# Kernel tuning notes

Measured on AMD Instinct MI355X. Metric: run time of the kernel, lower is better.

Reference implementation:

```python
import jax, jax.numpy as jnp
import numpy as np

VALUES_PER_ITEM = 4  # 2-bit packed -> 4 values per uint8


def setup_inputs() -> dict:
    key = jax.random.key(0)
    k1, k2, k3 = jax.random.split(key, 3)
    x = jax.random.normal(k1, (4, 4096, 2048), dtype=jnp.float32)
    # packed uint8 weights, stored as int32 with values in [0, 256)
    weight_packed = jax.random.randint(k2, (512, 2048), 0, 256, dtype=jnp.int32)
    weight_scale = jnp.ones((1,), dtype=jnp.float32)
    bias = jax.random.normal(k3, (2048,), dtype=jnp.float32) * 0.01
    return {"x": x, "weight_packed": weight_packed,
            "weight_scale": weight_scale, "bias": bias}


def unpack_weights_bitnet(packed, dtype):
    # packed: [out//4, in]. HF BitNet layout: group i occupies rows
    # [i*out//4 : (i+1)*out//4], extracted from bits (2i, 2i+1), minus 1.
    parts = [((packed >> (2 * i)) & 3) for i in range(VALUES_PER_ITEM)]
    return jnp.concatenate(parts, axis=0).astype(dtype) - 1.0  # [out, in]


def activation_quant(x, num_bits=8):
    qn = -(2 ** (num_bits - 1))          # -128
    qp = 2 ** (num_bits - 1) - 1         # 127
    amax = jnp.clip(jnp.max(jnp.abs(x), axis=-1, keepdims=True), 1e-5, None)
    scale = qp / amax                    # per-token scale, [..., 1]
    # round-half-to-even matches torch .round(); keep in float (int8-valued)
    xq = jnp.clip(jnp.round(x * scale), qn, qp)
    return xq, scale


def reference(x, weight_packed, weight_scale, bias):
    w = unpack_weights_bitnet(weight_packed, x.dtype)  # [out, in]
    xq, in_scale = activation_quant(x)                 # [b,s,in], [b,s,1]
    y = jnp.einsum('bsd,od->bso', xq, w)               # int8-valued GEMM in fp
    y = y / (weight_scale * in_scale)                  # rescale
    return y + bias
```

## Files before the change

### kernel.cpp

```cpp
#include <hip/hip_runtime.h>
#include <hip/hip_bf16.h>
#include <stdint.h>


typedef __attribute__((ext_vector_type(4))) int int4v;

#define GLOBAL_AS __attribute__((address_space(1)))
#define LDS_AS    __attribute__((address_space(3)))

static constexpr int MK = 2048;
static constexpr int NN = 2048;
static constexpr int MM = 16384;

__global__ void quant_kernel(const float* __restrict__ x,
                             const float* __restrict__ wscale,
                             signed char* __restrict__ xq,
                             float* __restrict__ rf) {
    const int m = blockIdx.x;
    const int t = threadIdx.x;
    const float4* xr = (const float4*)(x + (size_t)m * MK);
    float4 v0 = xr[t];
    float4 v1 = xr[t + 256];
    float amax = fmaxf(fmaxf(fabsf(v0.x), fabsf(v0.y)),
                       fmaxf(fabsf(v0.z), fabsf(v0.w)));
    amax = fmaxf(amax, fmaxf(fmaxf(fabsf(v1.x), fabsf(v1.y)),
                             fmaxf(fabsf(v1.z), fabsf(v1.w))));
    #pragma unroll
    for (int off = 32; off >= 1; off >>= 1)
        amax = fmaxf(amax, __shfl_xor(amax, off));
    __shared__ float smax[4];
    if ((t & 63) == 0) smax[t >> 6] = amax;
    __syncthreads();
    float a0 = fmaxf(fmaxf(smax[0], smax[1]), fmaxf(smax[2], smax[3]));
    a0 = fmaxf(a0, 1e-5f);
    const float scale = 127.0f / a0;
    if (t == 0) rf[m] = a0 / (127.0f * wscale[0]);

    auto q = [&](float f) -> int {
        float r = rintf(f * scale);
        r = fminf(fmaxf(r, -128.0f), 127.0f);
        return (int)r;
    };
    int p0 = (q(v0.x) & 255) | ((q(v0.y) & 255) << 8) |
             ((q(v0.z) & 255) << 16) | ((q(v0.w) & 255) << 24);
    int p1 = (q(v1.x) & 255) | ((q(v1.y) & 255) << 8) |
             ((q(v1.z) & 255) << 16) | ((q(v1.w) & 255) << 24);
    int* xqr = (int*)(xq + (size_t)m * MK);
    xqr[t]       = p0;
    xqr[t + 256] = p1;
}

__global__ void unpack_kernel(const int* __restrict__ packed,
                              signed char* __restrict__ W) {
    const int idx = blockIdx.x * 256 + threadIdx.x;
    const int r  = idx >> 9;
    const int kq = idx & 511;
    const int4 p = ((const int4*)packed)[idx];
    int* Wi = (int*)W;
    #pragma unroll
    for (int i = 0; i < 4; i++) {
        const int sh = 2 * i;
        int b0 = ((((p.x >> sh) & 3) - 1) & 255);
        int b1 = ((((p.y >> sh) & 3) - 1) & 255);
        int b2 = ((((p.z >> sh) & 3) - 1) & 255);
        int b3 = ((((p.w >> sh) & 3) - 1) & 255);
        Wi[(i * 512 + r) * 512 + kq] = b0 | (b1 << 8) | (b2 << 16) | (b3 << 24);
    }
}

__global__ void __launch_bounds__(256)
gemm_kernel(const signed char* __restrict__ xq,
            const signed char* __restrict__ W,
            const float* __restrict__ rf,
            const float* __restrict__ bias,
            float* __restrict__ out) {
    constexpr int BK = 64;
    __shared__ __attribute__((aligned(16))) unsigned char As[128 * BK];
    __shared__ __attribute__((aligned(16))) unsigned char Bs[128 * BK];

    const int tid  = threadIdx.x;
    const int wave = tid >> 6;
    const int lane = tid & 63;
    const int m0 = blockIdx.y * 128;
    const int n0 = blockIdx.x * 128;

    const int srow  = lane >> 2;
    const int sbyte = ((lane & 3) ^ ((srow >> 1) & 3)) * 16;

    const int wm = (wave >> 1) * 64;
    const int wn = (wave & 1) * 64;
    const int fr = lane & 15;
    const int fslot = ((lane >> 4) ^ ((fr >> 1) & 3)) * 16;

    int4v acc[4][4] = {};

    for (int k0 = 0; k0 < MK; k0 += BK) {
        #pragma unroll
        for (int c = 2 * wave; c < 2 * wave + 2; c++) {
            const signed char* ga =
                xq + (size_t)(m0 + c * 16 + srow) * MK + k0 + sbyte;
            __builtin_amdgcn_global_load_lds((const GLOBAL_AS void*)ga,
                                             (LDS_AS void*)(As + c * 1024),
                                             16, 0, 0);
            const signed char* gb =
                W + (size_t)(n0 + c * 16 + srow) * MK + k0 + sbyte;
            __builtin_amdgcn_global_load_lds((const GLOBAL_AS void*)gb,
                                             (LDS_AS void*)(Bs + c * 1024),
                                             16, 0, 0);
        }
        __syncthreads();

        int4v af[4], bf[4];
        #pragma unroll
        for (int i = 0; i < 4; i++) {
            af[i] = *(const int4v*)(As + (wm + i * 16 + fr) * BK + fslot);
            bf[i] = *(const int4v*)(Bs + (wn + i * 16 + fr) * BK + fslot);
        }
        #pragma unroll
        for (int mt = 0; mt < 4; mt++)
            #pragma unroll
            for (int nt = 0; nt < 4; nt++)
                acc[mt][nt] = __builtin_amdgcn_mfma_i32_16x16x64_i8(
                    af[mt], bf[nt], acc[mt][nt], 0, 0, 0);
        __syncthreads();
    }

    const int col   = lane & 15;
    const int rbase = (lane >> 4) * 4;
    #pragma unroll
    for (int mt = 0; mt < 4; mt++) {
        #pragma unroll
        for (int r = 0; r < 4; r++) {
            const int m = m0 + wm + mt * 16 + rbase + r;
            const float rfm = rf[m];
            #pragma unroll
            for (int nt = 0; nt < 4; nt++) {
                const int n = n0 + wn + nt * 16 + col;
                out[(size_t)m * NN + n] = (float)acc[mt][nt][r] * rfm + bias[n];
            }
        }
    }
}

extern "C" void kernel_launch(void* const* d_in, const int* in_sizes, int n_in,
                              void* d_out, int out_size, void* d_ws, size_t ws_size,
                              hipStream_t stream) {
    const float* x      = (const float*)d_in[0];
    const int*   packed = (const int*)d_in[1];
    const float* wscale = (const float*)d_in[2];
    const float* bias   = (const float*)d_in[3];
    float* out = (float*)d_out;

    signed char* xq = (signed char*)d_ws;
    signed char* W  = xq + (size_t)MM * MK;
    float*       rf = (float*)(W + (size_t)NN * MK);

    quant_kernel<<<MM, 256, 0, stream>>>(x, wscale, xq, rf);
    unpack_kernel<<<(512 * 512) / 256, 256, 0, stream>>>(packed, W);
    gemm_kernel<<<dim3(NN / 128, MM / 128), 256, 0, stream>>>(xq, W, rf, bias, out);
}
```

Before: 312.6 us.

## Rewrite int8 GEMM with 256x256 tiles, double-buffered LDS and phased MFMA pipeline

Replaces the 128x128, single-buffered int8 MFMA GEMM with a 512-thread 256x256 tile kernel. It uses 128-wide K steps, double-buffered 128KB LDS and asynchronous global-to-LDS loads interleaved with four compute phases using explicit vmcnt waits and priority hints. It also swizzles block order for L2 locality, and hoists bias loads in the epilogue. It aims to hide load latency and raise MFMA utilization, at the cost of heavy LDS use and fragile hand-tuned wait counts.

```diff
diff --git a/kernel.cpp b/kernel.cpp
--- a/kernel.cpp
+++ b/kernel.cpp
@@ -1,5 +1,4 @@
 #include <hip/hip_runtime.h>
-#include <hip/hip_bf16.h>
 #include <stdint.h>
 
 
@@ -68,76 +67,128 @@
     }
 }
 
-__global__ void __launch_bounds__(256)
+#define WAITV(N) asm volatile("s_waitcnt vmcnt(" #N ")" ::: "memory")
+
+__device__ __forceinline__ void stage_half(const signed char* __restrict__ src,
+                                           int row0, int k0, int h, int ss,
+                                           unsigned char* plane,
+                                           int wave, int lane) {
+    const int csrc = (((lane & 7) ^ (lane >> 3)) << 4);
+    #pragma unroll
+    for (int j = 0; j < 2; ++j) {
+        const int rw = wave * 16 + j * 8 + (lane >> 3);
+        const int r  = (rw & ((1 << ss) - 1)) + (h << ss)
+                     + ((rw >> ss) << (ss + 1));
+        const signed char* ga = src + (size_t)(row0 + r) * MK + k0 + csrc;
+        __builtin_amdgcn_global_load_lds((const GLOBAL_AS void*)ga,
+            (LDS_AS void*)(plane + (h << 14) + (wave * 2 + j) * 1024),
+            16, 0, 0);
+    }
+}
+
+#define PH(MH, NH, DO_READA, STAGE, WAIT)                                      \
+  do {                                                                         \
+    if (DO_READA) {                                                            \
+      _Pragma("unroll")                                                        \
+      for (int mt = 0; mt < 4; ++mt) {                                         \
+        a[mt][0] = *(const int4v*)(shp + cb + aoff0 + (MH)*16384 + mt*2048);   \
+        a[mt][1] = *(const int4v*)(shp + cb + aoff1 + (MH)*16384 + mt*2048);   \
+      }                                                                        \
+    }                                                                          \
+    _Pragma("unroll")                                                          \
+    for (int nf = 0; nf < 2; ++nf) {                                           \
+      b[nf][0] = *(const int4v*)(shp + cb + boff0 + (NH)*16384 + nf*2048);     \
+      b[nf][1] = *(const int4v*)(shp + cb + boff1 + (NH)*16384 + nf*2048);     \
+    }                                                                          \
+    STAGE;                                                                     \
+    WAIT;                                                                      \
+    __builtin_amdgcn_s_barrier();                                              \
+    __builtin_amdgcn_sched_barrier(0);                                         \
+    __builtin_amdgcn_s_setprio(1);                                             \
+    _Pragma("unroll")                                                          \
+    for (int mt = 0; mt < 4; ++mt) {                                           \
+      _Pragma("unroll")                                                        \
+      for (int nf = 0; nf < 2; ++nf) {                                         \
+        acc[(MH)*4+mt][(NH)*2+nf] = __builtin_amdgcn_mfma_i32_16x16x64_i8(     \
+            a[mt][0], b[nf][0], acc[(MH)*4+mt][(NH)*2+nf], 0, 0, 0);           \
+        acc[(MH)*4+mt][(NH)*2+nf] = __builtin_amdgcn_mfma_i32_16x16x64_i8(     \
+            a[mt][1], b[nf][1], acc[(MH)*4+mt][(NH)*2+nf], 0, 0, 0);           \
+      }                                                                        \
+    }                                                                          \
+    __builtin_amdgcn_s_setprio(0);                                             \
+  } while (0)
+
+__global__ void __launch_bounds__(512, 2)
 gemm_kernel(const signed char* __restrict__ xq,
             const signed char* __restrict__ W,
             const float* __restrict__ rf,
             const float* __restrict__ bias,
             float* __restrict__ out) {
-    constexpr int BK = 64;
-    __shared__ __attribute__((aligned(16))) unsigned char As[128 * BK];
-    __shared__ __attribute__((aligned(16))) unsigned char Bs[128 * BK];
+    __shared__ __attribute__((aligned(16))) unsigned char sh[131072];
+    unsigned char* shp = sh;
 
     const int tid  = threadIdx.x;
     const int wave = tid >> 6;
     const int lane = tid & 63;
-    const int m0 = blockIdx.y * 128;
-    const int n0 = blockIdx.x * 128;
-
-    const int srow  = lane >> 2;
-    const int sbyte = ((lane & 3) ^ ((srow >> 1) & 3)) * 16;
-
-    const int wm = (wave >> 1) * 64;
-    const int wn = (wave & 1) * 64;
-    const int fr = lane & 15;
-    const int fslot = ((lane >> 4) ^ ((fr >> 1) & 3)) * 16;
-
-    int4v acc[4][4] = {};
-
-    for (int k0 = 0; k0 < MK; k0 += BK) {
+    const int wm = wave >> 2;
+    const int wn = wave & 3;
+
+    const int bs = ((blockIdx.x & 7) << 6) | (blockIdx.x >> 3);
+    const int m0 = (bs >> 3) << 8;
+    const int n0 = (bs & 7) << 8;
+
+    const int fr = lane & 15, lq = lane >> 4, f7 = fr & 7;
+    const int cks0  = (lq ^ f7) << 4;
+    const int aoff0 = (wm * 64 + fr) * 128 + cks0;
+    const int aoff1 = aoff0 ^ 64;
+    const int boff0 = 32768 + (wn * 32 + fr) * 128 + cks0;
+    const int boff1 = boff0 ^ 64;
+
+    int4v a[4][2], b[2][2];
+    int4v acc[8][4] = {};
+
+    stage_half(xq, m0, 0, 0, 6, shp,        wave, lane);
+    stage_half(W,  n0, 0, 0, 5, shp + 32768, wave, lane);
+    stage_half(W,  n0, 0, 1, 5, shp + 32768, wave, lane);
+    stage_half(xq, m0, 0, 1, 6, shp,        wave, lane);
+    WAITV(4);
+    __builtin_amdgcn_s_barrier();
+    __builtin_amdgcn_sched_barrier(0);
+
+    #pragma unroll 1
+    for (int t = 0; t < 15; ++t) {
+        const int cb = (t & 1) << 16;
+        const int nb = cb ^ 65536;
+        const int k1 = (t + 1) << 7;
+        PH(0, 0, 1, stage_half(xq, m0, k1, 0, 6, shp + nb,        wave, lane), WAITV(4));
+        PH(0, 1, 0, stage_half(W,  n0, k1, 0, 5, shp + nb + 32768, wave, lane), WAITV(4));
+        PH(1, 0, 1, stage_half(W,  n0, k1, 1, 5, shp + nb + 32768, wave, lane), WAITV(6));
+        PH(1, 1, 0, stage_half(xq, m0, k1, 1, 6, shp + nb,        wave, lane), WAITV(4));
+    }
+    {
+        const int cb = 65536;
+        PH(0, 0, 1, (void)0, WAITV(2));
+        PH(0, 1, 0, (void)0, WAITV(0));
+        PH(1, 0, 1, (void)0, (void)0);
+        PH(1, 1, 0, (void)0, (void)0);
+    }
+
+    const int col = lane & 15;
+    const int rq  = (lane >> 4) * 4;
+    const int nbase = n0 + wn * 64 + col;
+    float bv[4];
+    #pragma unroll
+    for (int nf = 0; nf < 4; ++nf) bv[nf] = bias[nbase + nf * 16];
+    #pragma unroll
+    for (int mf = 0; mf < 8; ++mf) {
         #pragma unroll
-        for (int c = 2 * wave; c < 2 * wave + 2; c++) {
-            const signed char* ga =
-                xq + (size_t)(m0 + c * 16 + srow) * MK + k0 + sbyte;
-            __builtin_amdgcn_global_load_lds((const GLOBAL_AS void*)ga,
-                                             (LDS_AS void*)(As + c * 1024),
-                                             16, 0, 0);
-            const signed char* gb =
-                W + (size_t)(n0 + c * 16 + srow) * MK + k0 + sbyte;
-            __builtin_amdgcn_global_load_lds((const GLOBAL_AS void*)gb,
-                                             (LDS_AS void*)(Bs + c * 1024),
-                                             16, 0, 0);
-        }
-        __syncthreads();
-
-        int4v af[4], bf[4];
-        #pragma unroll
-        for (int i = 0; i < 4; i++) {
-            af[i] = *(const int4v*)(As + (wm + i * 16 + fr) * BK + fslot);
-            bf[i] = *(const int4v*)(Bs + (wn + i * 16 + fr) * BK + fslot);
-        }
-        #pragma unroll
-        for (int mt = 0; mt < 4; mt++)
+        for (int rr = 0; rr < 4; ++rr) {
+            const int m = m0 + wm * 128 + mf * 16 + rq + rr;
+            const float frm = rf[m];
+            float* orow = out + (size_t)m * NN;
             #pragma unroll
-            for (int nt = 0; nt < 4; nt++)
-                acc[mt][nt] = __builtin_amdgcn_mfma_i32_16x16x64_i8(
-                    af[mt], bf[nt], acc[mt][nt], 0, 0, 0);
-        __syncthreads();
-    }
-
-    const int col   = lane & 15;
-    const int rbase = (lane >> 4) * 4;
-    #pragma unroll
-    for (int mt = 0; mt < 4; mt++) {
-        #pragma unroll
-        for (int r = 0; r < 4; r++) {
-            const int m = m0 + wm + mt * 16 + rbase + r;
-            const float rfm = rf[m];
-            #pragma unroll
-            for (int nt = 0; nt < 4; nt++) {
-                const int n = n0 + wn + nt * 16 + col;
-                out[(size_t)m * NN + n] = (float)acc[mt][nt][r] * rfm + bias[n];
-            }
+            for (int nf = 0; nf < 4; ++nf)
+                orow[nbase + nf * 16] = (float)acc[mf][nf][rr] * frm + bv[nf];
         }
     }
 }
@@ -157,5 +208,5 @@
 
     quant_kernel<<<MM, 256, 0, stream>>>(x, wscale, xq, rf);
     unpack_kernel<<<(512 * 512) / 256, 256, 0, stream>>>(packed, W);
-    gemm_kernel<<<dim3(NN / 128, MM / 128), 256, 0, stream>>>(xq, W, rf, bias, out);
-}
+    gemm_kernel<<<dim3(512), 512, 0, stream>>>(xq, W, rf, bias, out);
+}
```

New measurement: 289.1 us. 7.5% less time.
